# Performance work log

Hardware: AMD Instinct MI355X
Metric: run time of the kernel (lower is better)

Reference implementation:

```python
import jax, jax.numpy as jnp
import numpy as np

C_CURV = 1.0
SQRT_C = C_CURV ** 0.5
MAX_NORM = 1.0 / SQRT_C - 1e-5  # project eps == dist clamp eps == 1e-5
EPS = 1e-15


def setup_inputs() -> dict:
    key = jax.random.key(0)
    k1, k2 = jax.random.split(key)
    B, C, D = 4096, 8192, 256
    # points well inside the unit ball: ||x|| ~ 0.05*sqrt(D) ~ 0.8
    x = jax.random.normal(k1, (B, D), dtype=jnp.float32) * 0.05
    # matches nn.Parameter(torch.randn(C, D) * 0.01)
    proto_tangent = jax.random.normal(k2, (C, D), dtype=jnp.float32) * 0.01
    log_scale = jnp.zeros((C,), dtype=jnp.float32)
    return {"x": x, "proto_tangent": proto_tangent, "log_scale": log_scale}


def _expmap0_project(v):
    # exp_0(v) = tanh(sqrt(c)||v||) v / (sqrt(c)||v||), then project onto ball
    vn = jnp.maximum(jnp.linalg.norm(v, axis=-1, keepdims=True), EPS)
    p = jnp.tanh(SQRT_C * vn) * v / (SQRT_C * vn)
    pn = jnp.linalg.norm(p, axis=-1, keepdims=True)
    return jnp.where(pn > MAX_NORM, p / pn * MAX_NORM, p)


def reference(x, proto_tangent, log_scale):
    protos = _expmap0_project(proto_tangent)          # [C, D]
    c = C_CURV
    # mobius_add(-x, y) broadcast over [B, C]; we only need its norm, so use
    # ||a*(-x) + b*y||^2 = a^2||x||^2 - 2ab<x,y> + b^2||y||^2 (same math,
    # avoids materializing the [B, C, D] intermediate the torch code builds).
    x2 = jnp.sum(x * x, axis=-1)[:, None]             # [B, 1]
    y2 = jnp.sum(protos * protos, axis=-1)[None, :]   # [1, C]
    xy = x @ protos.T                                  # [B, C]  <x, y>
    nxy = -xy                                          # <-x, y>
    a = 1.0 + 2.0 * c * nxy + c * y2                   # coeff of (-x)
    b = 1.0 - c * x2                                   # coeff of y
    denom = jnp.maximum(1.0 + 2.0 * c * nxy + (c * c) * x2 * y2, EPS)
    num_sq = a * a * x2 + 2.0 * a * b * nxy + b * b * y2
    norm = jnp.sqrt(jnp.maximum(num_sq, 0.0)) / denom  # ||mobius_add(-x,y)||
    # project clamp (eps=1e-5) and dist clamp (1/sqrt(c)-1e-5) coincide
    norm = jnp.minimum(norm, MAX_NORM)
    dists = (2.0 / SQRT_C) * jnp.arctanh(SQRT_C * norm)  # [B, C]
    return -dists * jnp.exp(log_scale)[None, :]
```

## Files before the change

kernel.cpp:

```cpp
#include <hip/hip_runtime.h>
#include <hip/hip_bf16.h>
#include <cstdint>

#define MAX_NORM (1.0f - 1e-5f)
#define LN2 0.69314718056f
#define WMAX ((1.0f + MAX_NORM) / (1.0f - MAX_NORM))

typedef __attribute__((ext_vector_type(8))) short bf16x8;
typedef __attribute__((ext_vector_type(4))) float f32x4;

__device__ __forceinline__ unsigned short f2bf(float f) {
  union { float f; unsigned int u; } c; c.f = f;
  unsigned int r = c.u + 0x7fffu + ((c.u >> 16) & 1u);
  return (unsigned short)(r >> 16);
}

__device__ __forceinline__ void gld16(const unsigned short* g, unsigned short* l) {
  __builtin_amdgcn_global_load_lds(
      (const __attribute__((address_space(1))) unsigned int*)g,
      (__attribute__((address_space(3))) unsigned int*)l, 16, 0, 0);
}

__global__ void prep_all(const float* __restrict__ x, const float* __restrict__ pt,
                         const float* __restrict__ ls,
                         unsigned short* __restrict__ xbf, unsigned short* __restrict__ pbf,
                         float* __restrict__ x2, float* __restrict__ fx,
                         float* __restrict__ gy, float* __restrict__ hy,
                         float* __restrict__ es2, int M, int N, int D) {
  int row = blockIdx.x * (blockDim.x >> 6) + (threadIdx.x >> 6);
  int lane = threadIdx.x & 63;
  if (row >= M + N) return;
  const bool isX = row < M;
  const int r = isX ? row : row - M;
  const float* src = (isX ? x : pt) + (size_t)r * D;
  f32x4 v = ((const f32x4*)src)[lane];
  float ss = v[0]*v[0] + v[1]*v[1] + v[2]*v[2] + v[3]*v[3];
  #pragma unroll
  for (int off = 32; off >= 1; off >>= 1) ss += __shfl_xor(ss, off);
  float scale = 1.0f;
  float outsq = ss;
  if (!isX) {
    float vn  = sqrtf(ss);
    float vnc = fmaxf(vn, 1e-15f);
    float th  = tanhf(vnc);
    scale = th / vnc;
    float pn = scale * vn;
    if (pn > MAX_NORM) { float pr = MAX_NORM / pn; scale *= pr; pn = MAX_NORM; }
    outsq = pn * pn;
  }
  unsigned short* dst = (isX ? xbf : pbf) + (size_t)r * D + lane * 4;
  unsigned long long pk =
        (unsigned long long)f2bf(v[0]*scale)
      | ((unsigned long long)f2bf(v[1]*scale) << 16)
      | ((unsigned long long)f2bf(v[2]*scale) << 32)
      | ((unsigned long long)f2bf(v[3]*scale) << 48);
  *(unsigned long long*)dst = pk;
  if (lane == 0) {
    if (isX) {
      x2[r] = outsq;
      fx[r] = 2.0f / (1.0f - outsq);
    } else {
      float g = 1.0f / (1.0f - outsq);
      gy[r]  = g;
      hy[r]  = g * outsq;
      es2[r] = -__expf(ls[r]) * LN2;
    }
  }
}

__global__ __launch_bounds__(256, 2)
void hyp_gemm(const unsigned short* __restrict__ xbf,
              const unsigned short* __restrict__ pbf,
              const float* __restrict__ x2, const float* __restrict__ fx,
              const float* __restrict__ gy, const float* __restrict__ hy,
              const float* __restrict__ es2, float* __restrict__ out,
              int M, int N, int K) {
  __shared__ __align__(16) unsigned short As[2][2][128 * 32];
  __shared__ __align__(16) unsigned short Bs[2][2][128 * 32];
  const int t    = threadIdx.x;
  const int wv   = t >> 6;
  const int lane = t & 63;
  const int wr   = wv >> 1, wc = wv & 1;
  const int frow = lane & 15, kgrp = lane >> 4;
  const int nTM  = M >> 7;
  const int tileM  = blockIdx.x % nTM;
  const int tileN0 = (blockIdx.x / nTM) * 4;
  const int gr0 = tileM * 128 + wr * 64;

  f32x4 accA[4][4], accB[4][4];

  const int srow  = wv * 16 + (lane >> 2);
  const int skoff = (lane & 3) * 8;
  const unsigned short* gA  = xbf + (size_t)(tileM * 128 + srow) * K + skoff;
  const unsigned short* gB0 = pbf + (size_t)(tileN0 * 128 + srow) * K + skoff;
  const size_t rskip = (size_t)64 * K;
  const size_t nskip = (size_t)128 * K;

  float x2s[4], fxs[4];
  #pragma unroll
  for (int m = 0; m < 4; ++m) {
    x2s[m] = x2[gr0 + m * 16 + frow];
    fxs[m] = fx[gr0 + m * 16 + frow];
  }

#define STAGE(b, kt, GBP)                                                      \
  {                                                                            \
    _Pragma("unroll")                                                          \
    for (int p = 0; p < 2; ++p) {                                              \
      _Pragma("unroll")                                                        \
      for (int j = 0; j < 2; ++j) {                                            \
        gld16(gA + (size_t)j * rskip + (kt) * 64 + p * 32,                     \
              &As[b][p][(j * 64 + wv * 16) * 32]);                             \
        gld16((GBP) + (size_t)j * rskip + (kt) * 64 + p * 32,                  \
              &Bs[b][p][(j * 64 + wv * 16) * 32]);                             \
      }                                                                        \
    }                                                                          \
  }

#define COMPUTE(b, ACC)                                                        \
  {                                                                            \
    __builtin_amdgcn_s_setprio(1);                                             \
    _Pragma("unroll")                                                          \
    for (int p = 0; p < 2; ++p) {                                              \
      bf16x8 af[4], bg[4];                                                     \
      _Pragma("unroll")                                                        \
      for (int m = 0; m < 4; ++m)                                              \
        af[m] = *(const bf16x8*)&As[b][p][(wr * 64 + m * 16 + frow) * 32 + kgrp * 8]; \
      _Pragma("unroll")                                                        \
      for (int n = 0; n < 4; ++n)                                              \
        bg[n] = *(const bf16x8*)&Bs[b][p][(wc * 64 + n * 16 + frow) * 32 + kgrp * 8]; \
      _Pragma("unroll")                                                        \
      for (int m = 0; m < 4; ++m)                                              \
        _Pragma("unroll")                                                      \
        for (int n = 0; n < 4; ++n)                                            \
          ACC[m][n] = __builtin_amdgcn_mfma_f32_16x16x32_bf16(bg[n], af[m], ACC[m][n], 0, 0, 0); \
    }                                                                          \
    __builtin_amdgcn_s_setprio(0);                                             \
  }

#define EPI_PAIR(ACC, TNP, NNP)                                                \
  {                                                                            \
    const int c0 = (tileN0 + (TNP)) * 128 + wc * 64 + (NNP) * 32 + kgrp * 4;   \
    f32x4 gv0 = *(const f32x4*)(gy  + c0);                                     \
    f32x4 hv0 = *(const f32x4*)(hy  + c0);                                     \
    f32x4 ev0 = *(const f32x4*)(es2 + c0);                                     \
    f32x4 gv1 = *(const f32x4*)(gy  + c0 + 16);                                \
    f32x4 hv1 = *(const f32x4*)(hy  + c0 + 16);                                \
    f32x4 ev1 = *(const f32x4*)(es2 + c0 + 16);                                \
    _Pragma("unroll")                                                          \
    for (int m = 0; m < 4; ++m) {                                              \
      f32x4 a0 = ACC[m][2 * (NNP)];                                            \
      f32x4 a1 = ACC[m][2 * (NNP) + 1];                                        \
      f32x4 o0, o1;                                                            \
      _Pragma("unroll")                                                        \
      for (int r = 0; r < 4; ++r) {                                            \
        float u0  = fmaf(fxs[m], fmaf(gv0[r], fmaf(-2.0f, a0[r], x2s[m]), hv0[r]), 1.0f); \
        float t20 = fmaxf(fmaf(u0, u0, -1.0f), 0.0f);                          \
        float w0  = fminf(u0 + __builtin_amdgcn_sqrtf(t20), WMAX);             \
        o0[r] = ev0[r] * __log2f(w0);                                          \
        float u1  = fmaf(fxs[m], fmaf(gv1[r], fmaf(-2.0f, a1[r], x2s[m]), hv1[r]), 1.0f); \
        float t21 = fmaxf(fmaf(u1, u1, -1.0f), 0.0f);                          \
        float w1  = fminf(u1 + __builtin_amdgcn_sqrtf(t21), WMAX);             \
        o1[r] = ev1[r] * __log2f(w1);                                          \
      }                                                                        \
      float* po = &out[(size_t)(gr0 + m * 16 + frow) * N + c0];                \
      *(f32x4*)po        = o0;                                                 \
      *(f32x4*)(po + 16) = o1;                                                 \
    }                                                                          \
  }

#define TILE(TN, ACCC, ACCP)                                                   \
  {                                                                            \
    _Pragma("unroll")                                                          \
    for (int m = 0; m < 4; ++m)                                                \
      _Pragma("unroll")                                                        \
      for (int n = 0; n < 4; ++n) ACCC[m][n] = (f32x4){0.f, 0.f, 0.f, 0.f};    \
    __syncthreads();                                                           \
    _Pragma("unroll")                                                          \
    for (int kt = 0; kt < 4; ++kt) {                                           \
      if (kt < 3)          STAGE(cur ^ 1, kt + 1, gB0 + (TN) * nskip)          \
      else if ((TN) < 3)   STAGE(cur ^ 1, 0, gB0 + ((TN) + 1) * nskip)         \
      if ((TN) > 0 && kt == 1) EPI_PAIR(ACCP, (TN) - 1, 0)                     \
      if ((TN) > 0 && kt == 3) EPI_PAIR(ACCP, (TN) - 1, 1)                     \
      COMPUTE(cur, ACCC)                                                       \
      __syncthreads();                                                         \
      cur ^= 1;                                                                \
    }                                                                          \
  }

  STAGE(0, 0, gB0)
  int cur = 0;
  TILE(0, accA, accB)
  TILE(1, accB, accA)
  TILE(2, accA, accB)
  TILE(3, accB, accA)
  EPI_PAIR(accB, 3, 0)
  EPI_PAIR(accB, 3, 1)

#undef TILE
#undef EPI_PAIR
#undef COMPUTE
#undef STAGE
}

extern "C" void kernel_launch(void* const* d_in, const int* in_sizes, int n_in,
                              void* d_out, int out_size, void* d_ws, size_t ws_size,
                              hipStream_t stream) {
  const float* x  = (const float*)d_in[0];
  const float* pt = (const float*)d_in[1];
  const float* ls = (const float*)d_in[2];
  const int Csz = in_sizes[2];
  const int D   = in_sizes[1] / Csz;
  const int Bsz = in_sizes[0] / D;
  const int M = Bsz, N = Csz, K = D;
  float* outp = (float*)d_out;

  char* ws = (char*)d_ws;
  unsigned short* xbf = (unsigned short*)ws; ws += (size_t)M * K * 2;
  unsigned short* pbf = (unsigned short*)ws; ws += (size_t)N * K * 2;
  float* x2  = (float*)ws; ws += (size_t)M * 4;
  float* fx  = (float*)ws; ws += (size_t)M * 4;
  float* gy  = (float*)ws; ws += (size_t)N * 4;
  float* hy  = (float*)ws; ws += (size_t)N * 4;
  float* es2 = (float*)ws; ws += (size_t)N * 4;

  hipLaunchKernelGGL(prep_all, dim3((M + N + 3) / 4), dim3(256), 0, stream,
                     x, pt, ls, xbf, pbf, x2, fx, gy, hy, es2, M, N, K);
  hipLaunchKernelGGL(hyp_gemm, dim3((M / 128) * (N / 512)), dim3(256), 0, stream,
                     xbf, pbf, x2, fx, gy, hy, es2, outp, M, N, K);
}
```

Measured before the change: 52.71 us.

## Keep A tile fragments resident in registers and drop double accumulator pipelining

The x (A) fragments for the whole K=256 are now loaded once from global memory into registers, which removes A's LDS staging, its shared memory and the A-side LDS reads across the four N tiles. It also drops the ping-pong accumulators, so each tile's epilogue runs after its MFMA loop instead of being interleaved with the next tile's compute. This frees the second accumulator set but adds 32 bf16x8 A fragment registers per thread. It also loses the overlap of the transcendental-heavy epilogue with matrix work, and the A fragments are read from global with strided per-row accesses.

Result: slower. 54.09 us (+2.6%).

```diff
diff --git a/kernel.cpp b/kernel.cpp
--- a/kernel.cpp
+++ b/kernel.cpp
@@ -75,7 +75,6 @@
               const float* __restrict__ gy, const float* __restrict__ hy,
               const float* __restrict__ es2, float* __restrict__ out,
               int M, int N, int K) {
-  __shared__ __align__(16) unsigned short As[2][2][128 * 32];
   __shared__ __align__(16) unsigned short Bs[2][2][128 * 32];
   const int t    = threadIdx.x;
   const int wv   = t >> 6;
@@ -87,11 +86,18 @@
   const int tileN0 = (blockIdx.x / nTM) * 4;
   const int gr0 = tileM * 128 + wr * 64;
 
-  f32x4 accA[4][4], accB[4][4];
+  f32x4 acc[4][4];
+
+  bf16x8 afr[4][8];
+  #pragma unroll
+  for (int m = 0; m < 4; ++m)
+    #pragma unroll
+    for (int s = 0; s < 8; ++s)
+      afr[m][s] = *(const bf16x8*)(xbf + (size_t)(gr0 + m * 16 + frow) * K
+                                   + s * 32 + kgrp * 8);
 
   const int srow  = wv * 16 + (lane >> 2);
   const int skoff = (lane & 3) * 8;
-  const unsigned short* gA  = xbf + (size_t)(tileM * 128 + srow) * K + skoff;
   const unsigned short* gB0 = pbf + (size_t)(tileN0 * 128 + srow) * K + skoff;
   const size_t rskip = (size_t)64 * K;
   const size_t nskip = (size_t)128 * K;
@@ -103,29 +109,24 @@
     fxs[m] = fx[gr0 + m * 16 + frow];
   }
 
-#define STAGE(b, kt, GBP)                                                      \
+#define STAGE_B(b, kt, GBP)                                                    \
   {                                                                            \
     _Pragma("unroll")                                                          \
     for (int p = 0; p < 2; ++p) {                                              \
       _Pragma("unroll")                                                        \
       for (int j = 0; j < 2; ++j) {                                            \
-        gld16(gA + (size_t)j * rskip + (kt) * 64 + p * 32,                     \
-              &As[b][p][(j * 64 + wv * 16) * 32]);                             \
         gld16((GBP) + (size_t)j * rskip + (kt) * 64 + p * 32,                  \
               &Bs[b][p][(j * 64 + wv * 16) * 32]);                             \
       }                                                                        \
     }                                                                          \
   }
 
-#define COMPUTE(b, ACC)                                                        \
+#define COMPUTE(b, KT)                                                         \
   {                                                                            \
     __builtin_amdgcn_s_setprio(1);                                             \
     _Pragma("unroll")                                                          \
     for (int p = 0; p < 2; ++p) {                                              \
-      bf16x8 af[4], bg[4];                                                     \
-      _Pragma("unroll")                                                        \
-      for (int m = 0; m < 4; ++m)                                              \
-        af[m] = *(const bf16x8*)&As[b][p][(wr * 64 + m * 16 + frow) * 32 + kgrp * 8]; \
+      bf16x8 bg[4];                                                            \
       _Pragma("unroll")                                                        \
       for (int n = 0; n < 4; ++n)                                              \
         bg[n] = *(const bf16x8*)&Bs[b][p][(wc * 64 + n * 16 + frow) * 32 + kgrp * 8]; \
@@ -133,12 +134,13 @@
       for (int m = 0; m < 4; ++m)                                              \
         _Pragma("unroll")                                                      \
         for (int n = 0; n < 4; ++n)                                            \
-          ACC[m][n] = __builtin_amdgcn_mfma_f32_16x16x32_bf16(bg[n], af[m], ACC[m][n], 0, 0, 0); \
+          acc[m][n] = __builtin_amdgcn_mfma_f32_16x16x32_bf16(                 \
+              bg[n], afr[m][(KT) * 2 + p], acc[m][n], 0, 0, 0);                \
     }                                                                          \
     __builtin_amdgcn_s_setprio(0);                                             \
   }
 
-#define EPI_PAIR(ACC, TNP, NNP)                                                \
+#define EPI_PAIR(TNP, NNP)                                                     \
   {                                                                            \
     const int c0 = (tileN0 + (TNP)) * 128 + wc * 64 + (NNP) * 32 + kgrp * 4;   \
     f32x4 gv0 = *(const f32x4*)(gy  + c0);                                     \
@@ -149,8 +151,8 @@
     f32x4 ev1 = *(const f32x4*)(es2 + c0 + 16);                                \
     _Pragma("unroll")                                                          \
     for (int m = 0; m < 4; ++m) {                                              \
-      f32x4 a0 = ACC[m][2 * (NNP)];                                            \
-      f32x4 a1 = ACC[m][2 * (NNP) + 1];                                        \
+      f32x4 a0 = acc[m][2 * (NNP)];                                            \
+      f32x4 a1 = acc[m][2 * (NNP) + 1];                                        \
       f32x4 o0, o1;                                                            \
       _Pragma("unroll")                                                        \
       for (int r = 0; r < 4; ++r) {                                            \
@@ -169,38 +171,36 @@
     }                                                                          \
   }
 
-#define TILE(TN, ACCC, ACCP)                                                   \
+#define TILE(TN)                                                               \
   {                                                                            \
     _Pragma("unroll")                                                          \
     for (int m = 0; m < 4; ++m)                                                \
       _Pragma("unroll")                                                        \
-      for (int n = 0; n < 4; ++n) ACCC[m][n] = (f32x4){0.f, 0.f, 0.f, 0.f};    \
+      for (int n = 0; n < 4; ++n) acc[m][n] = (f32x4){0.f, 0.f, 0.f, 0.f};     \
     __syncthreads();                                                           \
     _Pragma("unroll")                                                          \
     for (int kt = 0; kt < 4; ++kt) {                                           \
-      if (kt < 3)          STAGE(cur ^ 1, kt + 1, gB0 + (TN) * nskip)          \
-      else if ((TN) < 3)   STAGE(cur ^ 1, 0, gB0 + ((TN) + 1) * nskip)         \
-      if ((TN) > 0 && kt == 1) EPI_PAIR(ACCP, (TN) - 1, 0)                     \
-      if ((TN) > 0 && kt == 3) EPI_PAIR(ACCP, (TN) - 1, 1)                     \
-      COMPUTE(cur, ACCC)                                                       \
+      if (kt < 3) STAGE_B(cur ^ 1, kt + 1, gB0 + (TN) * nskip)                 \
+      COMPUTE(cur, kt)                                                         \
       __syncthreads();                                                         \
       cur ^= 1;                                                                \
     }                                                                          \
-  }
-
-  STAGE(0, 0, gB0)
+    if ((TN) < 3) STAGE_B(cur, 0, gB0 + ((TN) + 1) * nskip)                    \
+    EPI_PAIR(TN, 0)                                                            \
+    EPI_PAIR(TN, 1)                                                            \
+  }
+
+  STAGE_B(0, 0, gB0)
   int cur = 0;
-  TILE(0, accA, accB)
-  TILE(1, accB, accA)
-  TILE(2, accA, accB)
-  TILE(3, accB, accA)
-  EPI_PAIR(accB, 3, 0)
-  EPI_PAIR(accB, 3, 1)
+  TILE(0)
+  TILE(1)
+  TILE(2)
+  TILE(3)
 
 #undef TILE
 #undef EPI_PAIR
 #undef COMPUTE
-#undef STAGE
+#undef STAGE_B
 }
 
 extern "C" void kernel_launch(void* const* d_in, const int* in_sizes, int n_in,
```
